# Performance work log

Hardware: AMD Instinct MI355X
Metric: run time of the kernel (lower is better)

## Reference

```python
import jax, jax.numpy as jnp
import numpy as np

DIM = 768
MID = 256
HEADS = 12
P_SCALE = 0.8
SCALE = (DIM // HEADS) ** -0.5


def setup_inputs() -> dict:
    key = jax.random.key(0)
    ks = jax.random.split(key, 9)
    B, N, C = 64, 197, DIM
    s = 0.02
    return {
        "x": jax.random.normal(ks[0], (B, N, C), jnp.float32),
        "qkv_w": jax.random.normal(ks[1], (3 * C, C), jnp.float32) * s,
        "qkv_b": jax.random.normal(ks[2], (3 * C,), jnp.float32) * s,
        "proj_w": jax.random.normal(ks[3], (C, C), jnp.float32) * s,
        "proj_b": jax.random.normal(ks[4], (C,), jnp.float32) * s,
        "down_w": jax.random.normal(ks[5], (MID, C), jnp.float32) * s,
        "down_b": jax.random.normal(ks[6], (MID,), jnp.float32) * s,
        "up_w": jax.random.normal(ks[7], (2 * C, MID), jnp.float32) * s,
        "up_b": jax.random.normal(ks[8], (2 * C,), jnp.float32) * s,
    }


def reference(x, qkv_w, qkv_b, proj_w, proj_b, down_w, down_b, up_w, up_b):
    B, N, C = x.shape
    H, D = HEADS, C // HEADS
    # Adapter: down -> tanh -> up gives kv prefix; q prefix is zeros
    kv_prefix = jnp.tanh(x @ down_w.T + down_b) @ up_w.T + up_b  # [B,N,2C]
    prefix = jnp.concatenate([jnp.zeros((B, N, C), x.dtype), kv_prefix], -1)
    qkv = (x @ qkv_w.T + qkv_b) + P_SCALE * prefix  # [B,N,3C]
    qkv = qkv.reshape(B, N, 3, H, D).transpose(2, 0, 3, 1, 4)  # [3,B,H,N,D]
    q, k, v = qkv[0], qkv[1], qkv[2]
    attn = jax.nn.softmax(jnp.einsum("bhnd,bhmd->bhnm", q, k) * SCALE, axis=-1)
    out = jnp.einsum("bhnm,bhmd->bhnd", attn, v)  # [B,H,N,D]
    out = out.transpose(0, 2, 1, 3).reshape(B, N, C)
    return out @ proj_w.T + proj_b
```

## Files before the change

### kernel.cpp

```cpp
#include <hip/hip_runtime.h>
#include <hip/hip_bf16.h>
#include <stdint.h>

#define DIM   768
#define MID   256
#define HEADS 12
#define NB    64
#define NN    197
#define NT    (NB*NN)
#define QKVC  2304
#define NCOMB 2560

typedef __attribute__((ext_vector_type(4))) float f32x4;
typedef __attribute__((ext_vector_type(8))) short s8v;

__device__ __forceinline__ unsigned short f2b(float f) {
    union { float f; unsigned int u; } x; x.f = f;
    unsigned int u = x.u;
    unsigned int r = (u + 0x7FFFu + ((u >> 16) & 1u)) >> 16;
    return (unsigned short)r;
}
__device__ __forceinline__ float b2f(unsigned short s) {
    union { unsigned int u; float f; } x; x.u = ((unsigned int)s) << 16;
    return x.f;
}

__device__ __forceinline__ void gld_lds16(const void* g, void* l) {
    __builtin_amdgcn_global_load_lds(
        (const __attribute__((address_space(1))) unsigned int*)g,
        (__attribute__((address_space(3))) unsigned int*)l, 16, 0, 0);
}

__global__ void cast_all(const float* __restrict__ x,
                         const float* __restrict__ qkv_w,
                         const float* __restrict__ down_w,
                         const float* __restrict__ up_w,
                         const float* __restrict__ proj_w,
                         unsigned short* __restrict__ xb,
                         unsigned short* __restrict__ o_comb,
                         unsigned short* __restrict__ o_up,
                         unsigned short* __restrict__ o_proj) {
    int blk = blockIdx.x;
    if (blk < 2048) {
        const int n4 = NT * DIM / 4;
        for (int i = blk * 256 + threadIdx.x; i < n4; i += 2048 * 256) {
            float4 v = ((const float4*)x)[i];
            ushort4 o;
            o.x = f2b(v.x); o.y = f2b(v.y); o.z = f2b(v.z); o.w = f2b(v.w);
            ((ushort4*)xb)[i] = o;
        }
        return;
    }
    blk -= 2048;
    const float* in; unsigned short* out; int base;
    if (blk < 1728)      { in = qkv_w;  out = o_comb;              base = blk; }
    else if (blk < 1920) { in = down_w; out = o_comb + QKVC * DIM; base = blk - 1728; }
    else if (blk < 2304) { in = up_w;   out = o_up;                base = blk - 1920; }
    else                 { in = proj_w; out = o_proj;              base = blk - 2304; }
    int i = base * 256 + threadIdx.x;
    float4 v = ((const float4*)in)[i];
    ushort4 o;
    o.x = f2b(v.x); o.y = f2b(v.y); o.z = f2b(v.z); o.w = f2b(v.w);
    ((ushort4*)out)[i] = o;
}

template<int EPI>
__global__ __launch_bounds__(256) void gemm_bt(
    const unsigned short* __restrict__ A,
    const unsigned short* __restrict__ W,
    const float* __restrict__ bias0,
    const float* __restrict__ bias1,
    int M, int K, int GN,
    unsigned short* __restrict__ ob0,
    unsigned short* __restrict__ ob1,
    float* __restrict__ outf)
{
    __shared__ __align__(16) unsigned short lds[3][2][128 * 32];
    const int tid = threadIdx.x;
    const int l = tid & 63;
    const int w = tid >> 6;
    const int wr = w >> 1, wc = w & 1;

    const int nwg = gridDim.x;
    const int orig = blockIdx.x;
    const int q8 = nwg >> 3, r8 = nwg & 7;
    const int xcd = orig & 7, slice = orig >> 3;
    const int wgid = (xcd < r8 ? xcd * (q8 + 1)
                               : r8 * (q8 + 1) + (xcd - r8) * q8) + slice;
    const int bm = wgid / GN;
    const int bn = wgid - bm * GN;

    f32x4 acc[4][4];
#pragma unroll
    for (int m = 0; m < 4; ++m)
#pragma unroll
        for (int n = 0; n < 4; ++n)
            acc[m][n] = (f32x4){0.f, 0.f, 0.f, 0.f};

    const int KT = K >> 5;

    const int src = (((tid & 3) ^ ((tid >> 3) & 3)) << 3);
    const int dst = ((tid & 3) << 3);
    const int dA0 = (tid >> 2) * 32 + dst;
    const int dA1 = dA0 + 64 * 32;
    int ra0 = bm * 128 + (tid >> 2);      if (ra0 > M - 1) ra0 = M - 1;
    int ra1 = bm * 128 + 64 + (tid >> 2); if (ra1 > M - 1) ra1 = M - 1;
    const int rb0 = bn * 128 + (tid >> 2);
    const int rb1 = rb0 + 64;
    const unsigned short* pa0 = A + (size_t)ra0 * K + src;
    const unsigned short* pa1 = A + (size_t)ra1 * K + src;
    const unsigned short* pb0 = W + (size_t)rb0 * K + src;
    const unsigned short* pb1 = W + (size_t)rb1 * K + src;

    auto stage = [&](int buf) {
        gld_lds16(pa0, &lds[buf][0][dA0]);
        gld_lds16(pb0, &lds[buf][1][dA0]);
        gld_lds16(pa1, &lds[buf][0][dA1]);
        gld_lds16(pb1, &lds[buf][1][dA1]);
        pa0 += 32; pa1 += 32; pb0 += 32; pb1 += 32;
    };

    stage(0);
    stage(1);

    const int rsl = (((l >> 4) ^ ((l >> 1) & 3)) << 3);
    int cb = 0;
    int sb = 2;
    for (int kt = 0; kt < KT; ++kt) {
        if (kt + 1 < KT) asm volatile("s_waitcnt vmcnt(4)" ::: "memory");
        else             asm volatile("s_waitcnt vmcnt(0)" ::: "memory");
        __builtin_amdgcn_s_barrier();
        asm volatile("" ::: "memory");
        if (kt + 2 < KT) stage(sb);
        const unsigned short* la = lds[cb][0];
        const unsigned short* lb = lds[cb][1];
        s8v a[4], b[4];
#pragma unroll
        for (int m = 0; m < 4; ++m)
            a[m] = *(const s8v*)&la[(wr * 64 + m * 16 + (l & 15)) * 32 + rsl];
#pragma unroll
        for (int n = 0; n < 4; ++n)
            b[n] = *(const s8v*)&lb[(wc * 64 + n * 16 + (l & 15)) * 32 + rsl];
        __builtin_amdgcn_s_setprio(1);
#pragma unroll
        for (int m = 0; m < 4; ++m)
#pragma unroll
            for (int n = 0; n < 4; ++n)
                acc[m][n] = __builtin_amdgcn_mfma_f32_16x16x32_bf16(a[m], b[n], acc[m][n], 0, 0, 0);
        __builtin_amdgcn_s_setprio(0);
        cb = (cb == 2) ? 0 : cb + 1;
        sb = (sb == 2) ? 0 : sb + 1;
    }
    __syncthreads();

    if (EPI == 0) {
        unsigned short* stg = ((unsigned short*)lds) + w * (16 * 68);
        const int C0 = bn * 128 + wc * 64;
        const bool ish = (C0 >= QKVC);
#pragma unroll
        for (int mq = 0; mq < 4; ++mq) {
#pragma unroll
            for (int n = 0; n < 4; ++n) {
                int c = C0 + n * 16 + (l & 15);
                float bi = ish ? bias1[c - QKVC] : bias0[c];
                float sc2 = (c < DIM) ? 0.125f : 1.0f;
#pragma unroll
                for (int j = 0; j < 4; ++j) {
                    float v = acc[mq][n][j] + bi;
                    v = ish ? tanhf(v) : v * sc2;
                    stg[((l >> 4) * 4 + j) * 68 + n * 16 + (l & 15)] = f2b(v);
                }
            }
#pragma unroll
            for (int p = 0; p < 2; ++p) {
                int rr2 = p * 8 + (l >> 3);
                int r = bm * 128 + wr * 64 + mq * 16 + rr2;
                s8v v = *(const s8v*)&stg[rr2 * 68 + (l & 7) * 8];
                if (r < M) {
                    if (!ish) *(s8v*)&ob0[(size_t)r * QKVC + C0 + (l & 7) * 8] = v;
                    else      *(s8v*)&ob1[(size_t)r * MID + (C0 - QKVC) + (l & 7) * 8] = v;
                }
            }
        }
    } else if (EPI == 1) {
        unsigned short* stg = ((unsigned short*)lds) + w * (16 * 68);
        const int C0 = bn * 128 + wc * 64;
#pragma unroll
        for (int mq = 0; mq < 4; ++mq) {
#pragma unroll
            for (int n = 0; n < 4; ++n) {
                int c = C0 + n * 16 + (l & 15);
                float bi = bias0[c];
#pragma unroll
                for (int j = 0; j < 4; ++j)
                    stg[((l >> 4) * 4 + j) * 68 + n * 16 + (l & 15)] =
                        f2b(0.8f * (acc[mq][n][j] + bi));
            }
#pragma unroll
            for (int p = 0; p < 2; ++p) {
                int rr2 = p * 8 + (l >> 3);
                int r = bm * 128 + wr * 64 + mq * 16 + rr2;
                if (r < M) {
                    size_t base = (size_t)r * QKVC + DIM + C0 + (l & 7) * 8;
                    s8v add = *(const s8v*)&stg[rr2 * 68 + (l & 7) * 8];
                    s8v old = *(const s8v*)&ob0[base];
                    s8v res;
#pragma unroll
                    for (int i = 0; i < 8; ++i)
                        res[i] = (short)f2b(b2f((unsigned short)old[i]) +
                                            b2f((unsigned short)add[i]));
                    *(s8v*)&ob0[base] = res;
                }
            }
        }
    } else {
#pragma unroll
        for (int n = 0; n < 4; ++n) {
            int c = bn * 128 + wc * 64 + n * 16 + (l & 15);
            float bi = bias0[c];
#pragma unroll
            for (int m = 0; m < 4; ++m) {
#pragma unroll
                for (int j = 0; j < 4; ++j) {
                    int r = bm * 128 + wr * 64 + m * 16 + (l >> 4) * 4 + j;
                    if (r >= M) continue;
                    outf[(size_t)r * DIM + c] = acc[m][n][j] + bi;
                }
            }
        }
    }
}

#define NKV  224
#define VPAD 232

__global__ __launch_bounds__(256) void attn_kernel(
    const unsigned short* __restrict__ qkv,
    unsigned short* __restrict__ ob)
{
    __shared__ __align__(16) unsigned short Ks[NKV * 64];
    __shared__ __align__(16) unsigned short Vt[64 * VPAD];
    __shared__ __align__(16) unsigned short Ps[64 * VPAD];

    const int tid = threadIdx.x;
    const int l = tid & 63;
    const int w = tid >> 6;
    const int bh = blockIdx.x;
    const int b = bh / HEADS, h = bh - b * HEADS;
    const unsigned short* qp = qkv + (size_t)(b * NN) * QKVC + h * 64;
    const unsigned short* kp = qp + DIM;
    const unsigned short* vp = qp + 2 * DIM;

    const s8v zer = (s8v){0, 0, 0, 0, 0, 0, 0, 0};

    for (int e = tid; e < NKV * 8; e += 256) {
        int r = e >> 3, ch = e & 7;
        int idx = (r * 64 + ch * 8) ^ ((r & 7) << 3);
        s8v val = (r < NN) ? *(const s8v*)&kp[(size_t)r * QKVC + ch * 8] : zer;
        *(s8v*)&Ks[idx] = val;
    }
    for (int e = tid; e < NKV * 8; e += 256) {
        int r = e >> 3, ch = e & 7;
        s8v val = (r < NN) ? *(const s8v*)&vp[(size_t)r * QKVC + ch * 8] : zer;
#pragma unroll
        for (int i = 0; i < 8; ++i)
            Vt[(ch * 8 + i) * VPAD + r] = (unsigned short)val[i];
    }
    __syncthreads();

    for (int qc = 0; qc < 4; ++qc) {
        const int rbase = qc * 64 + w * 16;
        s8v aq[2];
#pragma unroll
        for (int kc = 0; kc < 2; ++kc) {
            int r = rbase + (l & 15); if (r > NN - 1) r = NN - 1;
            aq[kc] = *(const s8v*)&qp[(size_t)r * QKVC + kc * 32 + (l >> 4) * 8];
        }
        f32x4 sacc[14];
#pragma unroll
        for (int t = 0; t < 14; ++t) sacc[t] = (f32x4){0.f, 0.f, 0.f, 0.f};
#pragma unroll
        for (int t = 0; t < 14; ++t) {
            int col = t * 16 + (l & 15);
#pragma unroll
            for (int kc = 0; kc < 2; ++kc) {
                int idx = (col * 64 + kc * 32 + (l >> 4) * 8) ^ ((col & 7) << 3);
                s8v bk = *(const s8v*)&Ks[idx];
                sacc[t] = __builtin_amdgcn_mfma_f32_16x16x32_bf16(aq[kc], bk, sacc[t], 0, 0, 0);
            }
        }
        float mx[4] = {-1e30f, -1e30f, -1e30f, -1e30f};
#pragma unroll
        for (int t = 0; t < 14; ++t) {
            int col = t * 16 + (l & 15);
            if (col < NN) {
#pragma unroll
                for (int j = 0; j < 4; ++j) mx[j] = fmaxf(mx[j], sacc[t][j]);
            }
        }
#pragma unroll
        for (int j = 0; j < 4; ++j)
#pragma unroll
            for (int off = 1; off < 16; off <<= 1)
                mx[j] = fmaxf(mx[j], __shfl_xor(mx[j], off, 64));

        float sm[4] = {0.f, 0.f, 0.f, 0.f};
#pragma unroll
        for (int t = 0; t < 14; ++t) {
            int col = t * 16 + (l & 15);
#pragma unroll
            for (int j = 0; j < 4; ++j) {
                float p = (col < NN) ? __expf(sacc[t][j] - mx[j]) : 0.f;
                sm[j] += p;
                Ps[(w * 16 + (l >> 4) * 4 + j) * VPAD + col] = f2b(p);
            }
        }
#pragma unroll
        for (int j = 0; j < 4; ++j)
#pragma unroll
            for (int off = 1; off < 16; off <<= 1)
                sm[j] += __shfl_xor(sm[j], off, 64);

        f32x4 oacc[4];
#pragma unroll
        for (int n = 0; n < 4; ++n) oacc[n] = (f32x4){0.f, 0.f, 0.f, 0.f};
#pragma unroll
        for (int kc = 0; kc < 7; ++kc) {
            s8v ap = *(const s8v*)&Ps[(w * 16 + (l & 15)) * VPAD + kc * 32 + (l >> 4) * 8];
#pragma unroll
            for (int n = 0; n < 4; ++n) {
                s8v bv = *(const s8v*)&Vt[(n * 16 + (l & 15)) * VPAD + kc * 32 + (l >> 4) * 8];
                oacc[n] = __builtin_amdgcn_mfma_f32_16x16x32_bf16(ap, bv, oacc[n], 0, 0, 0);
            }
        }
#pragma unroll
        for (int n = 0; n < 4; ++n) {
#pragma unroll
            for (int j = 0; j < 4; ++j) {
                int r = rbase + (l >> 4) * 4 + j;
                if (r < NN) {
                    float val = oacc[n][j] / sm[j];
                    ob[((size_t)(b * NN + r)) * DIM + h * 64 + n * 16 + (l & 15)] = f2b(val);
                }
            }
        }
    }
}

extern "C" void kernel_launch(void* const* d_in, const int* in_sizes, int n_in,
                              void* d_out, int out_size, void* d_ws, size_t ws_size,
                              hipStream_t stream) {
    const float* x      = (const float*)d_in[0];
    const float* qkv_w  = (const float*)d_in[1];
    const float* qkv_b  = (const float*)d_in[2];
    const float* proj_w = (const float*)d_in[3];
    const float* proj_b = (const float*)d_in[4];
    const float* down_w = (const float*)d_in[5];
    const float* down_b = (const float*)d_in[6];
    const float* up_w   = (const float*)d_in[7];
    const float* up_b   = (const float*)d_in[8];
    float* out = (float*)d_out;

    char* ws = (char*)d_ws;
    size_t off = 0;
    unsigned short* xb      = (unsigned short*)(ws + off); off += (size_t)NT * DIM * 2;
    unsigned short* wcomb   = (unsigned short*)(ws + off); off += (size_t)NCOMB * DIM * 2;
    unsigned short* up_wb   = (unsigned short*)(ws + off); off += (size_t)2 * DIM * MID * 2;
    unsigned short* proj_wb = (unsigned short*)(ws + off); off += (size_t)DIM * DIM * 2;
    unsigned short* hbuf    = (unsigned short*)(ws + off); off += (size_t)NT * MID * 2;
    unsigned short* qkvbuf  = (unsigned short*)(ws + off); off += (size_t)NT * QKVC * 2;
    unsigned short* obuf    = xb;

    cast_all<<<2048 + 2880, 256, 0, stream>>>(x, qkv_w, down_w, up_w, proj_w,
                                              xb, wcomb, up_wb, proj_wb);

    const int GM1 = (NT + 127) / 128;
    gemm_bt<0><<<GM1 * (NCOMB / 128), 256, 0, stream>>>(xb, wcomb, qkv_b, down_b,
                                                        NT, DIM, NCOMB / 128,
                                                        qkvbuf, hbuf, nullptr);
    gemm_bt<1><<<GM1 * (2 * DIM / 128), 256, 0, stream>>>(hbuf, up_wb, up_b, nullptr,
                                                          NT, MID, 2 * DIM / 128,
                                                          qkvbuf, nullptr, nullptr);
    attn_kernel<<<NB * HEADS, 256, 0, stream>>>(qkvbuf, obuf);
    gemm_bt<2><<<GM1 * (DIM / 128), 256, 0, stream>>>(obuf, proj_wb, proj_b, nullptr,
                                                      NT, DIM, DIM / 128,
                                                      nullptr, nullptr, out);
}
```

Baseline: 207.4 us.

## Use K=64 double-buffered GEMM tiles for the QKV and projection GEMMs

Adds a new GEMM variant that stages 64-wide K tiles into two LDS buffers instead of 32-wide tiles in three buffers. Each iteration issues the next tile's loads before computing two MFMA sub-steps, with an XOR swizzle sized for 64-column rows. This halves the number of barrier and wait round-trips per K and makes each global load batch larger. The small up-projection GEMM keeps the old three-buffer K=32 pipeline as a separate kernel. Doubling the LDS footprint per block may lower occupancy.

```diff
diff --git a/kernel.cpp b/kernel.cpp
--- a/kernel.cpp
+++ b/kernel.cpp
@@ -65,7 +65,7 @@
 }
 
 template<int EPI>
-__global__ __launch_bounds__(256) void gemm_bt(
+__global__ __launch_bounds__(256) void gemm64(
     const unsigned short* __restrict__ A,
     const unsigned short* __restrict__ W,
     const float* __restrict__ bias0,
@@ -75,7 +75,7 @@
     unsigned short* __restrict__ ob1,
     float* __restrict__ outf)
 {
-    __shared__ __align__(16) unsigned short lds[3][2][128 * 32];
+    __shared__ __align__(16) unsigned short lds[2][2][128 * 64];
     const int tid = threadIdx.x;
     const int l = tid & 63;
     const int w = tid >> 6;
@@ -97,6 +97,152 @@
         for (int n = 0; n < 4; ++n)
             acc[m][n] = (f32x4){0.f, 0.f, 0.f, 0.f};
 
+    const int KT = K >> 6;
+
+    const int sr = tid >> 3;
+    const int sc = tid & 7;
+    const int srco = ((sc ^ (sr & 7)) << 3);
+    const int dbase = sr * 64 + sc * 8;
+    int ra0 = bm * 128 +  0 + sr; if (ra0 > M - 1) ra0 = M - 1;
+    int ra1 = bm * 128 + 32 + sr; if (ra1 > M - 1) ra1 = M - 1;
+    int ra2 = bm * 128 + 64 + sr; if (ra2 > M - 1) ra2 = M - 1;
+    int ra3 = bm * 128 + 96 + sr; if (ra3 > M - 1) ra3 = M - 1;
+    const unsigned short* pa0 = A + (size_t)ra0 * K + srco;
+    const unsigned short* pa1 = A + (size_t)ra1 * K + srco;
+    const unsigned short* pa2 = A + (size_t)ra2 * K + srco;
+    const unsigned short* pa3 = A + (size_t)ra3 * K + srco;
+    const unsigned short* pb0 = W + (size_t)(bn * 128 +  0 + sr) * K + srco;
+    const unsigned short* pb1 = W + (size_t)(bn * 128 + 32 + sr) * K + srco;
+    const unsigned short* pb2 = W + (size_t)(bn * 128 + 64 + sr) * K + srco;
+    const unsigned short* pb3 = W + (size_t)(bn * 128 + 96 + sr) * K + srco;
+
+    auto stage = [&](int buf) {
+        gld_lds16(pa0, &lds[buf][0][dbase]);
+        gld_lds16(pa1, &lds[buf][0][dbase + 32 * 64]);
+        gld_lds16(pa2, &lds[buf][0][dbase + 64 * 64]);
+        gld_lds16(pa3, &lds[buf][0][dbase + 96 * 64]);
+        gld_lds16(pb0, &lds[buf][1][dbase]);
+        gld_lds16(pb1, &lds[buf][1][dbase + 32 * 64]);
+        gld_lds16(pb2, &lds[buf][1][dbase + 64 * 64]);
+        gld_lds16(pb3, &lds[buf][1][dbase + 96 * 64]);
+        pa0 += 64; pa1 += 64; pa2 += 64; pa3 += 64;
+        pb0 += 64; pb1 += 64; pb2 += 64; pb3 += 64;
+    };
+
+    stage(0);
+
+    const int ch0 = (((l >> 4)    ) ^ (l & 7)) << 3;
+    const int ch1 = (((l >> 4) + 4) ^ (l & 7)) << 3;
+    int buf = 0;
+    for (int kt = 0; kt < KT; ++kt) {
+        if (kt + 1 < KT) {
+            stage(buf ^ 1);
+            asm volatile("s_waitcnt vmcnt(8)" ::: "memory");
+        } else {
+            asm volatile("s_waitcnt vmcnt(0)" ::: "memory");
+        }
+        __builtin_amdgcn_s_barrier();
+        const unsigned short* la = lds[buf][0];
+        const unsigned short* lb = lds[buf][1];
+#pragma unroll
+        for (int kk = 0; kk < 2; ++kk) {
+            const int ch = kk ? ch1 : ch0;
+            s8v a[4], b[4];
+#pragma unroll
+            for (int m = 0; m < 4; ++m)
+                a[m] = *(const s8v*)&la[(wr * 64 + m * 16 + (l & 15)) * 64 + ch];
+#pragma unroll
+            for (int n = 0; n < 4; ++n)
+                b[n] = *(const s8v*)&lb[(wc * 64 + n * 16 + (l & 15)) * 64 + ch];
+            __builtin_amdgcn_s_setprio(1);
+#pragma unroll
+            for (int m = 0; m < 4; ++m)
+#pragma unroll
+                for (int n = 0; n < 4; ++n)
+                    acc[m][n] = __builtin_amdgcn_mfma_f32_16x16x32_bf16(a[m], b[n], acc[m][n], 0, 0, 0);
+            __builtin_amdgcn_s_setprio(0);
+        }
+        __builtin_amdgcn_s_barrier();
+        buf ^= 1;
+    }
+    __syncthreads();
+
+    if (EPI == 0) {
+        unsigned short* stg = ((unsigned short*)lds) + w * (16 * 68);
+        const int C0 = bn * 128 + wc * 64;
+        const bool ish = (C0 >= QKVC);
+#pragma unroll
+        for (int mq = 0; mq < 4; ++mq) {
+#pragma unroll
+            for (int n = 0; n < 4; ++n) {
+                int c = C0 + n * 16 + (l & 15);
+                float bi = ish ? bias1[c - QKVC] : bias0[c];
+                float sc2 = (c < DIM) ? 0.125f : 1.0f;
+#pragma unroll
+                for (int j = 0; j < 4; ++j) {
+                    float v = acc[mq][n][j] + bi;
+                    v = ish ? tanhf(v) : v * sc2;
+                    stg[((l >> 4) * 4 + j) * 68 + n * 16 + (l & 15)] = f2b(v);
+                }
+            }
+#pragma unroll
+            for (int p = 0; p < 2; ++p) {
+                int rr2 = p * 8 + (l >> 3);
+                int r = bm * 128 + wr * 64 + mq * 16 + rr2;
+                s8v v = *(const s8v*)&stg[rr2 * 68 + (l & 7) * 8];
+                if (r < M) {
+                    if (!ish) *(s8v*)&ob0[(size_t)r * QKVC + C0 + (l & 7) * 8] = v;
+                    else      *(s8v*)&ob1[(size_t)r * MID + (C0 - QKVC) + (l & 7) * 8] = v;
+                }
+            }
+        }
+    } else {
+#pragma unroll
+        for (int n = 0; n < 4; ++n) {
+            int c = bn * 128 + wc * 64 + n * 16 + (l & 15);
+            float bi = bias0[c];
+#pragma unroll
+            for (int m = 0; m < 4; ++m) {
+#pragma unroll
+                for (int j = 0; j < 4; ++j) {
+                    int r = bm * 128 + wr * 64 + m * 16 + (l >> 4) * 4 + j;
+                    if (r >= M) continue;
+                    outf[(size_t)r * DIM + c] = acc[m][n][j] + bi;
+                }
+            }
+        }
+    }
+}
+
+__global__ __launch_bounds__(256) void gemm_up(
+    const unsigned short* __restrict__ A,
+    const unsigned short* __restrict__ W,
+    const float* __restrict__ bias0,
+    int M, int K, int GN,
+    unsigned short* __restrict__ ob0)
+{
+    __shared__ __align__(16) unsigned short lds[3][2][128 * 32];
+    const int tid = threadIdx.x;
+    const int l = tid & 63;
+    const int w = tid >> 6;
+    const int wr = w >> 1, wc = w & 1;
+
+    const int nwg = gridDim.x;
+    const int orig = blockIdx.x;
+    const int q8 = nwg >> 3, r8 = nwg & 7;
+    const int xcd = orig & 7, slice = orig >> 3;
+    const int wgid = (xcd < r8 ? xcd * (q8 + 1)
+                               : r8 * (q8 + 1) + (xcd - r8) * q8) + slice;
+    const int bm = wgid / GN;
+    const int bn = wgid - bm * GN;
+
+    f32x4 acc[4][4];
+#pragma unroll
+    for (int m = 0; m < 4; ++m)
+#pragma unroll
+        for (int n = 0; n < 4; ++n)
+            acc[m][n] = (f32x4){0.f, 0.f, 0.f, 0.f};
+
     const int KT = K >> 5;
 
     const int src = (((tid & 3) ^ ((tid >> 3) & 3)) << 3);
@@ -105,12 +251,10 @@
     const int dA1 = dA0 + 64 * 32;
     int ra0 = bm * 128 + (tid >> 2);      if (ra0 > M - 1) ra0 = M - 1;
     int ra1 = bm * 128 + 64 + (tid >> 2); if (ra1 > M - 1) ra1 = M - 1;
-    const int rb0 = bn * 128 + (tid >> 2);
-    const int rb1 = rb0 + 64;
     const unsigned short* pa0 = A + (size_t)ra0 * K + src;
     const unsigned short* pa1 = A + (size_t)ra1 * K + src;
-    const unsigned short* pb0 = W + (size_t)rb0 * K + src;
-    const unsigned short* pb1 = W + (size_t)rb1 * K + src;
+    const unsigned short* pb0 = W + (size_t)(bn * 128 + (tid >> 2)) * K + src;
+    const unsigned short* pb1 = W + (size_t)(bn * 128 + 64 + (tid >> 2)) * K + src;
 
     auto stage = [&](int buf) {
         gld_lds16(pa0, &lds[buf][0][dA0]);
@@ -153,79 +297,33 @@
     }
     __syncthreads();
 
-    if (EPI == 0) {
-        unsigned short* stg = ((unsigned short*)lds) + w * (16 * 68);
-        const int C0 = bn * 128 + wc * 64;
-        const bool ish = (C0 >= QKVC);
-#pragma unroll
-        for (int mq = 0; mq < 4; ++mq) {
-#pragma unroll
-            for (int n = 0; n < 4; ++n) {
-                int c = C0 + n * 16 + (l & 15);
-                float bi = ish ? bias1[c - QKVC] : bias0[c];
-                float sc2 = (c < DIM) ? 0.125f : 1.0f;
-#pragma unroll
-                for (int j = 0; j < 4; ++j) {
-                    float v = acc[mq][n][j] + bi;
-                    v = ish ? tanhf(v) : v * sc2;
-                    stg[((l >> 4) * 4 + j) * 68 + n * 16 + (l & 15)] = f2b(v);
-                }
-            }
-#pragma unroll
-            for (int p = 0; p < 2; ++p) {
-                int rr2 = p * 8 + (l >> 3);
-                int r = bm * 128 + wr * 64 + mq * 16 + rr2;
-                s8v v = *(const s8v*)&stg[rr2 * 68 + (l & 7) * 8];
-                if (r < M) {
-                    if (!ish) *(s8v*)&ob0[(size_t)r * QKVC + C0 + (l & 7) * 8] = v;
-                    else      *(s8v*)&ob1[(size_t)r * MID + (C0 - QKVC) + (l & 7) * 8] = v;
-                }
-            }
-        }
-    } else if (EPI == 1) {
-        unsigned short* stg = ((unsigned short*)lds) + w * (16 * 68);
-        const int C0 = bn * 128 + wc * 64;
-#pragma unroll
-        for (int mq = 0; mq < 4; ++mq) {
-#pragma unroll
-            for (int n = 0; n < 4; ++n) {
-                int c = C0 + n * 16 + (l & 15);
-                float bi = bias0[c];
-#pragma unroll
-                for (int j = 0; j < 4; ++j)
-                    stg[((l >> 4) * 4 + j) * 68 + n * 16 + (l & 15)] =
-                        f2b(0.8f * (acc[mq][n][j] + bi));
-            }
-#pragma unroll
-            for (int p = 0; p < 2; ++p) {
-                int rr2 = p * 8 + (l >> 3);
-                int r = bm * 128 + wr * 64 + mq * 16 + rr2;
-                if (r < M) {
-                    size_t base = (size_t)r * QKVC + DIM + C0 + (l & 7) * 8;
-                    s8v add = *(const s8v*)&stg[rr2 * 68 + (l & 7) * 8];
-                    s8v old = *(const s8v*)&ob0[base];
-                    s8v res;
-#pragma unroll
-                    for (int i = 0; i < 8; ++i)
-                        res[i] = (short)f2b(b2f((unsigned short)old[i]) +
-                                            b2f((unsigned short)add[i]));
-                    *(s8v*)&ob0[base] = res;
-                }
-            }
-        }
-    } else {
+    unsigned short* stg = ((unsigned short*)lds) + w * (16 * 68);
+    const int C0 = bn * 128 + wc * 64;
+#pragma unroll
+    for (int mq = 0; mq < 4; ++mq) {
 #pragma unroll
         for (int n = 0; n < 4; ++n) {
-            int c = bn * 128 + wc * 64 + n * 16 + (l & 15);
+            int c = C0 + n * 16 + (l & 15);
             float bi = bias0[c];
 #pragma unroll
-            for (int m = 0; m < 4; ++m) {
-#pragma unroll
-                for (int j = 0; j < 4; ++j) {
-                    int r = bm * 128 + wr * 64 + m * 16 + (l >> 4) * 4 + j;
-                    if (r >= M) continue;
-                    outf[(size_t)r * DIM + c] = acc[m][n][j] + bi;
-                }
+            for (int j = 0; j < 4; ++j)
+                stg[((l >> 4) * 4 + j) * 68 + n * 16 + (l & 15)] =
+                    f2b(0.8f * (acc[mq][n][j] + bi));
+        }
+#pragma unroll
+        for (int p = 0; p < 2; ++p) {
+            int rr2 = p * 8 + (l >> 3);
+            int r = bm * 128 + wr * 64 + mq * 16 + rr2;
+            if (r < M) {
+                size_t base = (size_t)r * QKVC + DIM + C0 + (l & 7) * 8;
+                s8v add = *(const s8v*)&stg[rr2 * 68 + (l & 7) * 8];
+                s8v old = *(const s8v*)&ob0[base];
+                s8v res;
+#pragma unroll
+                for (int i = 0; i < 8; ++i)
+                    res[i] = (short)f2b(b2f((unsigned short)old[i]) +
+                                        b2f((unsigned short)add[i]));
+                *(s8v*)&ob0[base] = res;
             }
         }
     }
@@ -375,14 +473,13 @@
                                               xb, wcomb, up_wb, proj_wb);
 
     const int GM1 = (NT + 127) / 128;
-    gemm_bt<0><<<GM1 * (NCOMB / 128), 256, 0, stream>>>(xb, wcomb, qkv_b, down_b,
-                                                        NT, DIM, NCOMB / 128,
-                                                        qkvbuf, hbuf, nullptr);
-    gemm_bt<1><<<GM1 * (2 * DIM / 128), 256, 0, stream>>>(hbuf, up_wb, up_b, nullptr,
-                                                          NT, MID, 2 * DIM / 128,
-                                                          qkvbuf, nullptr, nullptr);
+    gemm64<0><<<GM1 * (NCOMB / 128), 256, 0, stream>>>(xb, wcomb, qkv_b, down_b,
+                                                       NT, DIM, NCOMB / 128,
+                                                       qkvbuf, hbuf, nullptr);
+    gemm_up<<<GM1 * (2 * DIM / 128), 256, 0, stream>>>(hbuf, up_wb, up_b, NT, MID, 2 * DIM / 128,
+                                                       qkvbuf);
     attn_kernel<<<NB * HEADS, 256, 0, stream>>>(qkvbuf, obuf);
-    gemm_bt<2><<<GM1 * (DIM / 128), 256, 0, stream>>>(obuf, proj_wb, proj_b, nullptr,
-                                                      NT, DIM, DIM / 128,
-                                                      nullptr, nullptr, out);
-}
+    gemm64<2><<<GM1 * (DIM / 128), 256, 0, stream>>>(obuf, proj_wb, proj_b, nullptr,
+                                                     NT, DIM, DIM / 128,
+                                                     nullptr, nullptr, out);
+}
```

New measurement: 218.6 us. 5.4% more time.
